# Performance work log

Measured on AMD Instinct MI355X. Metric: run time of the kernel, lower is better.

Reference implementation:

```python
import jax, jax.numpy as jnp
import numpy as np

H, R, B = 8192, 4, 64


def glorot(key, shape):
    return jax.random.uniform(key, shape, minval=-1.0, maxval=1.0) * jnp.sqrt(2.0 / sum(shape))


def setup_inputs() -> dict:
    key = jax.random.key(0)
    k1, k2, k3, k4, kh, kx = jax.random.split(key, 6)
    return {
        "h": jax.random.normal(kh, (B, H), dtype=jnp.float32),
        "x": jax.random.normal(kx, (B, H), dtype=jnp.float32),
        "a_diag": glorot(k1, (H,)).astype(jnp.float32),
        "p_vec": glorot(k2, (H, R)).astype(jnp.float32),
        "q_vec": glorot(k3, (H, R)).astype(jnp.float32),
        "b_mat": glorot(k4, (H, H)).astype(jnp.float32),
    }


def reference(h, x, a_diag, p_vec, q_vec, b_mat):
    # Faithful to the source: explicitly materialize the dense DPLR matrix
    # a_dplr = diag(a_diag) + p q^T  (H x H), then a_dplr @ h + b_mat.T @ x.
    a_dplr = jnp.diag(a_diag) + p_vec @ q_vec.T  # (H, H)
    # Batched over leading dim: (a_dplr @ h_i) == h @ a_dplr.T ; (b_mat.T @ x_i) == x @ b_mat
    return h @ a_dplr.T + x @ b_mat  # (B, H)
```

## Files before the change

kernel.cpp:

```cpp
#include <hip/hip_runtime.h>
#include <hip/hip_bf16.h>


#define HDIM 8192
#define BDIM 64
#define RDIM 4
#define KSPLIT 16
#define KSLAB 512
#define NKTILE (KSLAB / 32)

typedef short short8 __attribute__((ext_vector_type(8)));
typedef float f32x2 __attribute__((ext_vector_type(2)));
typedef float f32x4 __attribute__((ext_vector_type(4)));
typedef float f32x16 __attribute__((ext_vector_type(16)));

__device__ __forceinline__ unsigned f2bf(float f) {
  unsigned u = __float_as_uint(f);
  unsigned r = u + 0x7fffu + ((u >> 16) & 1u);
  return r >> 16;
}

__device__ __forceinline__ float bf2f(unsigned short u) {
  return __uint_as_float(((unsigned)u) << 16);
}

__global__ __launch_bounds__(256)
void prep_hq_kernel(const float* __restrict__ x,
                    const float* __restrict__ h,
                    const float* __restrict__ q,
                    unsigned short* __restrict__ xb,
                    float* __restrict__ hq) {
  const int b = blockIdx.x, t = threadIdx.x;
  {
    const float* xrow = x + (size_t)b * HDIM;
    unsigned short* xo = xb + (size_t)b * HDIM;
#pragma unroll
    for (int i = 0; i < 4; ++i) {
      const int base = (t * 4 + i) * 8;
      f32x4 v0 = *(const f32x4*)(xrow + base);
      f32x4 v1 = *(const f32x4*)(xrow + base + 4);
      union { unsigned short u[8]; short8 s; } o;
#pragma unroll
      for (int e = 0; e < 4; ++e) {
        o.u[e] = (unsigned short)f2bf(v0[e]);
        o.u[4 + e] = (unsigned short)f2bf(v1[e]);
      }
      *(short8*)(xo + base) = o.s;
    }
  }
  const float* hrow = h + (size_t)b * HDIM;
  f32x4 s = {0.f, 0.f, 0.f, 0.f};
  for (int k = t; k < HDIM; k += 256) {
    float hv = hrow[k];
    f32x4 qv = *(const f32x4*)(q + (size_t)k * RDIM);
    s += hv * qv;
  }
  __shared__ f32x4 red[256];
  red[t] = s;
  __syncthreads();
  for (int off = 128; off > 0; off >>= 1) {
    if (t < off) red[t] += red[t + off];
    __syncthreads();
  }
  if (t == 0) *(f32x4*)(hq + (size_t)b * RDIM) = red[0];
}

__global__ __launch_bounds__(512, 2)
void dplr_main(const float* __restrict__ bmat,
               const unsigned short* __restrict__ xb,
               unsigned short* __restrict__ part) {
  __shared__ __align__(16) unsigned short xs[BDIM * KSLAB];

  const int t    = threadIdx.x;
  const int lane = t & 63;
  const int w    = t >> 6;
  const int c32  = lane & 31;
  const int kh   = lane >> 5;

  const int jg = blockIdx.x & 15;
  const int ks = blockIdx.x >> 4;
  const int k0 = ks * KSLAB;

  {
    const int row = t >> 3;
    const int g0  = (t & 7) * 8;
    const unsigned short* src = xb + (size_t)row * HDIM + k0 + g0 * 8;
#pragma unroll
    for (int i = 0; i < 8; ++i) {
      const int g  = row * (KSLAB / 8) + g0 + i;
      const int gs = g ^ (row & 7);
      *(short8*)&xs[gs * 8] = *(const short8*)(src + i * 8);
    }
  }
  __syncthreads();

  const int j0 = jg * 512 + w * 64;
  const float* b0 = bmat + (size_t)(k0 + kh * 8) * HDIM + j0 + 2 * c32;

  f32x16 acc[2][2];
#pragma unroll
  for (int mt = 0; mt < 2; ++mt)
#pragma unroll
    for (int n = 0; n < 2; ++n)
#pragma unroll
      for (int r = 0; r < 16; ++r) acc[mt][n][r] = 0.f;

  f32x2 LA[16], LB[16], LC[16], LD[16];

  auto issue = [&](int kt, f32x2* L) {
#pragma unroll
    for (int s = 0; s < 2; ++s)
#pragma unroll
      for (int i = 0; i < 8; ++i)
        L[s * 8 + i] = *(const f32x2*)(b0 + (size_t)(kt * 32 + s * 16 + i) * HDIM);
  };

  auto conv_mfma = [&](int kt, const f32x2* L) {
#pragma unroll
    for (int s = 0; s < 2; ++s) {
      union { unsigned u[4]; short8 v; } bf0, bf1;
#pragma unroll
      for (int j = 0; j < 4; ++j) {
        const f32x2 a = L[s * 8 + 2 * j];
        const f32x2 b = L[s * 8 + 2 * j + 1];
        bf0.u[j] = f2bf(a.x) | (f2bf(b.x) << 16);
        bf1.u[j] = f2bf(a.y) | (f2bf(b.y) << 16);
      }
#pragma unroll
      for (int mt = 0; mt < 2; ++mt) {
        const int row = mt * 32 + c32;
        const int g   = row * (KSLAB / 8) + kt * 4 + s * 2 + kh;
        const int gs  = g ^ (row & 7);
        short8 af = *(const short8*)&xs[gs * 8];
        acc[mt][0] = __builtin_amdgcn_mfma_f32_32x32x16_bf16(af, bf0.v, acc[mt][0], 0, 0, 0);
        acc[mt][1] = __builtin_amdgcn_mfma_f32_32x32x16_bf16(af, bf1.v, acc[mt][1], 0, 0, 0);
      }
    }
  };

  issue(0, LA);
  issue(1, LB);
  issue(2, LC);
  issue(3, LD);
  for (int kt = 0; kt < NKTILE; kt += 4) {
    conv_mfma(kt, LA);
    if (kt + 4 < NKTILE) issue(kt + 4, LA);
    conv_mfma(kt + 1, LB);
    if (kt + 5 < NKTILE) issue(kt + 5, LB);
    conv_mfma(kt + 2, LC);
    if (kt + 6 < NKTILE) issue(kt + 6, LC);
    conv_mfma(kt + 3, LD);
    if (kt + 7 < NKTILE) issue(kt + 7, LD);
  }

  unsigned short* pb = part + (size_t)ks * BDIM * HDIM;
#pragma unroll
  for (int mt = 0; mt < 2; ++mt)
#pragma unroll
    for (int n = 0; n < 2; ++n)
#pragma unroll
      for (int reg = 0; reg < 16; ++reg) {
        const int row = mt * 32 + (reg & 3) + 8 * (reg >> 2) + 4 * kh;
        const int col = j0 + 2 * c32 + n;
        pb[(size_t)row * HDIM + col] = (unsigned short)f2bf(acc[mt][n][reg]);
      }
}

__global__ __launch_bounds__(256)
void combine_kernel(const unsigned short* __restrict__ part,
                    const float* __restrict__ h,
                    const float* __restrict__ adiag,
                    const float* __restrict__ pvec,
                    const float* __restrict__ hq,
                    float* __restrict__ out) {
  const int tid  = blockIdx.x * 256 + threadIdx.x;
  const int base = tid * 8;
  const int row  = base >> 13;
  const int j    = base & 8191;

  float s[8];
#pragma unroll
  for (int e = 0; e < 8; ++e) s[e] = 0.f;
  const unsigned short* pp = part + (size_t)row * HDIM + j;
#pragma unroll
  for (int ks = 0; ks < KSPLIT; ++ks) {
    union { unsigned short u[8]; short8 v; } pv;
    pv.v = *(const short8*)(pp + (size_t)ks * BDIM * HDIM);
#pragma unroll
    for (int e = 0; e < 8; ++e) s[e] += bf2f(pv.u[e]);
  }
  const f32x4 hv0 = *(const f32x4*)(h + (size_t)row * HDIM + j);
  const f32x4 hv1 = *(const f32x4*)(h + (size_t)row * HDIM + j + 4);
  const f32x4 a0  = *(const f32x4*)(adiag + j);
  const f32x4 a1  = *(const f32x4*)(adiag + j + 4);
  const f32x4 hqv = *(const f32x4*)(hq + (size_t)row * RDIM);

  float res[8];
#pragma unroll
  for (int e = 0; e < 4; ++e) {
    const f32x4 pv = *(const f32x4*)(pvec + (size_t)(j + e) * RDIM);
    res[e] = s[e] + hv0[e] * a0[e] +
             hqv[0] * pv[0] + hqv[1] * pv[1] + hqv[2] * pv[2] + hqv[3] * pv[3];
  }
#pragma unroll
  for (int e = 0; e < 4; ++e) {
    const f32x4 pv = *(const f32x4*)(pvec + (size_t)(j + 4 + e) * RDIM);
    res[4 + e] = s[4 + e] + hv1[e] * a1[e] +
                 hqv[0] * pv[0] + hqv[1] * pv[1] + hqv[2] * pv[2] + hqv[3] * pv[3];
  }
  f32x4 o0 = {res[0], res[1], res[2], res[3]};
  f32x4 o1 = {res[4], res[5], res[6], res[7]};
  *(f32x4*)(out + (size_t)row * HDIM + j) = o0;
  *(f32x4*)(out + (size_t)row * HDIM + j + 4) = o1;
}

extern "C" void kernel_launch(void* const* d_in, const int* in_sizes, int n_in,
                              void* d_out, int out_size, void* d_ws, size_t ws_size,
                              hipStream_t stream) {
  const float* h     = (const float*)d_in[0];
  const float* x     = (const float*)d_in[1];
  const float* adiag = (const float*)d_in[2];
  const float* pvec  = (const float*)d_in[3];
  const float* qvec  = (const float*)d_in[4];
  const float* bmat  = (const float*)d_in[5];
  float* out = (float*)d_out;

  unsigned short* xb = (unsigned short*)d_ws;
  float* hqbuf = (float*)((char*)d_ws + ((size_t)1 << 20));
  unsigned short* part = (unsigned short*)((char*)d_ws + ((size_t)2 << 20));

  prep_hq_kernel<<<BDIM, 256, 0, stream>>>(x, h, qvec, xb, hqbuf);
  dplr_main<<<KSPLIT * 16, 512, 0, stream>>>(bmat, xb, part);
  combine_kernel<<<(BDIM * HDIM / 8) / 256, 256, 0, stream>>>(part, h, adiag, pvec, hqbuf, out);
}
```

Before: 73.53 us.

## Widen B-tile per wave, convert x inside main kernel, double K-split

The main GEMM kernel now converts fp32 x to bf16 directly into shared memory, so the separate x-conversion pass and its workspace buffer go away. Each wave loads full 128-byte-per-lane-pair rows of b_mat and uses v_permlane32_swap to rearrange them into MFMA operands, covering 128 output columns with 4 accumulators instead of 64 with 2. K is split 32 ways with 256-deep slabs, keeping the grid at 256 blocks. The cost is twice as many partial-sum slabs for the combine kernel to read and more accumulator registers per wave.

```diff
diff --git a/kernel.cpp b/kernel.cpp
--- a/kernel.cpp
+++ b/kernel.cpp
@@ -5,9 +5,9 @@
 #define HDIM 8192
 #define BDIM 64
 #define RDIM 4
-#define KSPLIT 16
-#define KSLAB 512
-#define NKTILE (KSLAB / 32)
+#define KSPLIT 32
+#define KSLAB 256
+#define NSTEP (KSLAB / 16)
 
 typedef short short8 __attribute__((ext_vector_type(8)));
 typedef float f32x2 __attribute__((ext_vector_type(2)));
@@ -25,29 +25,10 @@
 }
 
 __global__ __launch_bounds__(256)
-void prep_hq_kernel(const float* __restrict__ x,
-                    const float* __restrict__ h,
-                    const float* __restrict__ q,
-                    unsigned short* __restrict__ xb,
-                    float* __restrict__ hq) {
+void hq_kernel(const float* __restrict__ h,
+               const float* __restrict__ q,
+               float* __restrict__ hq) {
   const int b = blockIdx.x, t = threadIdx.x;
-  {
-    const float* xrow = x + (size_t)b * HDIM;
-    unsigned short* xo = xb + (size_t)b * HDIM;
-#pragma unroll
-    for (int i = 0; i < 4; ++i) {
-      const int base = (t * 4 + i) * 8;
-      f32x4 v0 = *(const f32x4*)(xrow + base);
-      f32x4 v1 = *(const f32x4*)(xrow + base + 4);
-      union { unsigned short u[8]; short8 s; } o;
-#pragma unroll
-      for (int e = 0; e < 4; ++e) {
-        o.u[e] = (unsigned short)f2bf(v0[e]);
-        o.u[4 + e] = (unsigned short)f2bf(v1[e]);
-      }
-      *(short8*)(xo + base) = o.s;
-    }
-  }
   const float* hrow = h + (size_t)b * HDIM;
   f32x4 s = {0.f, 0.f, 0.f, 0.f};
   for (int k = t; k < HDIM; k += 256) {
@@ -67,7 +48,7 @@
 
 __global__ __launch_bounds__(512, 2)
 void dplr_main(const float* __restrict__ bmat,
-               const unsigned short* __restrict__ xb,
+               const float* __restrict__ x,
                unsigned short* __restrict__ part) {
   __shared__ __align__(16) unsigned short xs[BDIM * KSLAB];
 
@@ -77,93 +58,100 @@
   const int c32  = lane & 31;
   const int kh   = lane >> 5;
 
-  const int jg = blockIdx.x & 15;
-  const int ks = blockIdx.x >> 4;
+  const int jg = blockIdx.x & 7;
+  const int ks = blockIdx.x >> 3;
   const int k0 = ks * KSLAB;
 
   {
-    const int row = t >> 3;
-    const int g0  = (t & 7) * 8;
-    const unsigned short* src = xb + (size_t)row * HDIM + k0 + g0 * 8;
+    const int row  = t >> 3;
+    const int koff = (t & 7) * 32;
+    const float* src = x + (size_t)row * HDIM + k0 + koff;
+#pragma unroll
+    for (int i = 0; i < 4; ++i) {
+      f32x4 va = *(const f32x4*)(src + i * 8);
+      f32x4 vb = *(const f32x4*)(src + i * 8 + 4);
+      union { unsigned short u[8]; short8 s; } o;
+#pragma unroll
+      for (int e = 0; e < 4; ++e) {
+        o.u[e]     = (unsigned short)f2bf(va[e]);
+        o.u[4 + e] = (unsigned short)f2bf(vb[e]);
+      }
+      const int g  = row * (KSLAB / 8) + (t & 7) * 4 + i;
+      const int gs = g ^ (row & 7);
+      *(short8*)&xs[gs * 8] = o.s;
+    }
+  }
+  __syncthreads();
+
+  const int j0 = jg * 1024 + w * 128;
+  const float* b0 = bmat + (size_t)k0 * HDIM + j0 + 2 * lane;
+
+  f32x16 acc[2][4];
+#pragma unroll
+  for (int mt = 0; mt < 2; ++mt)
+#pragma unroll
+    for (int n = 0; n < 4; ++n)
+#pragma unroll
+      for (int r = 0; r < 16; ++r) acc[mt][n][r] = 0.f;
+
+  f32x2 LA[16], LB[16];
+
+  auto issue = [&](int kt, f32x2* L) {
+#pragma unroll
+    for (int i = 0; i < 16; ++i)
+      L[i] = *(const f32x2*)(b0 + (size_t)(kt * 16 + i) * HDIM);
+  };
+
+  auto consume = [&](int kt, f32x2* L) {
 #pragma unroll
     for (int i = 0; i < 8; ++i) {
-      const int g  = row * (KSLAB / 8) + g0 + i;
-      const int gs = g ^ (row & 7);
-      *(short8*)&xs[gs * 8] = *(const short8*)(src + i * 8);
-    }
-  }
-  __syncthreads();
-
-  const int j0 = jg * 512 + w * 64;
-  const float* b0 = bmat + (size_t)(k0 + kh * 8) * HDIM + j0 + 2 * c32;
-
-  f32x16 acc[2][2];
-#pragma unroll
-  for (int mt = 0; mt < 2; ++mt)
-#pragma unroll
-    for (int n = 0; n < 2; ++n)
-#pragma unroll
-      for (int r = 0; r < 16; ++r) acc[mt][n][r] = 0.f;
-
-  f32x2 LA[16], LB[16], LC[16], LD[16];
-
-  auto issue = [&](int kt, f32x2* L) {
-#pragma unroll
-    for (int s = 0; s < 2; ++s)
-#pragma unroll
-      for (int i = 0; i < 8; ++i)
-        L[s * 8 + i] = *(const f32x2*)(b0 + (size_t)(kt * 32 + s * 16 + i) * HDIM);
-  };
-
-  auto conv_mfma = [&](int kt, const f32x2* L) {
-#pragma unroll
-    for (int s = 0; s < 2; ++s) {
-      union { unsigned u[4]; short8 v; } bf0, bf1;
-#pragma unroll
-      for (int j = 0; j < 4; ++j) {
-        const f32x2 a = L[s * 8 + 2 * j];
-        const f32x2 b = L[s * 8 + 2 * j + 1];
-        bf0.u[j] = f2bf(a.x) | (f2bf(b.x) << 16);
-        bf1.u[j] = f2bf(a.y) | (f2bf(b.y) << 16);
-      }
-#pragma unroll
-      for (int mt = 0; mt < 2; ++mt) {
-        const int row = mt * 32 + c32;
-        const int g   = row * (KSLAB / 8) + kt * 4 + s * 2 + kh;
-        const int gs  = g ^ (row & 7);
-        short8 af = *(const short8*)&xs[gs * 8];
-        acc[mt][0] = __builtin_amdgcn_mfma_f32_32x32x16_bf16(af, bf0.v, acc[mt][0], 0, 0, 0);
-        acc[mt][1] = __builtin_amdgcn_mfma_f32_32x32x16_bf16(af, bf1.v, acc[mt][1], 0, 0, 0);
-      }
+      asm volatile("v_permlane32_swap_b32 %0, %1"
+                   : "+v"(L[i].x), "+v"(L[i + 8].x));
+      asm volatile("v_permlane32_swap_b32 %0, %1"
+                   : "+v"(L[i].y), "+v"(L[i + 8].y));
+    }
+    union { unsigned u[4]; short8 v; } bf[4];
+#pragma unroll
+    for (int j = 0; j < 4; ++j) {
+      bf[0].u[j] = f2bf(L[2 * j].x)     | (f2bf(L[2 * j + 1].x) << 16);
+      bf[1].u[j] = f2bf(L[2 * j].y)     | (f2bf(L[2 * j + 1].y) << 16);
+      bf[2].u[j] = f2bf(L[8 + 2 * j].x) | (f2bf(L[8 + 2 * j + 1].x) << 16);
+      bf[3].u[j] = f2bf(L[8 + 2 * j].y) | (f2bf(L[8 + 2 * j + 1].y) << 16);
+    }
+#pragma unroll
+    for (int mt = 0; mt < 2; ++mt) {
+      const int row = mt * 32 + c32;
+      const int g   = row * (KSLAB / 8) + kt * 2 + kh;
+      const int gs  = g ^ (row & 7);
+      short8 af = *(const short8*)&xs[gs * 8];
+#pragma unroll
+      for (int n = 0; n < 4; ++n)
+        acc[mt][n] =
+            __builtin_amdgcn_mfma_f32_32x32x16_bf16(af, bf[n].v, acc[mt][n], 0, 0, 0);
     }
   };
 
   issue(0, LA);
   issue(1, LB);
-  issue(2, LC);
-  issue(3, LD);
-  for (int kt = 0; kt < NKTILE; kt += 4) {
-    conv_mfma(kt, LA);
-    if (kt + 4 < NKTILE) issue(kt + 4, LA);
-    conv_mfma(kt + 1, LB);
-    if (kt + 5 < NKTILE) issue(kt + 5, LB);
-    conv_mfma(kt + 2, LC);
-    if (kt + 6 < NKTILE) issue(kt + 6, LC);
-    conv_mfma(kt + 3, LD);
-    if (kt + 7 < NKTILE) issue(kt + 7, LD);
+  for (int kt = 0; kt < NSTEP; kt += 2) {
+    consume(kt, LA);
+    if (kt + 2 < NSTEP) issue(kt + 2, LA);
+    consume(kt + 1, LB);
+    if (kt + 3 < NSTEP) issue(kt + 3, LB);
   }
 
   unsigned short* pb = part + (size_t)ks * BDIM * HDIM;
 #pragma unroll
   for (int mt = 0; mt < 2; ++mt)
 #pragma unroll
-    for (int n = 0; n < 2; ++n)
+    for (int n = 0; n < 4; ++n) {
+      const int col = j0 + ((n >> 1) * 64) + 2 * c32 + (n & 1);
 #pragma unroll
       for (int reg = 0; reg < 16; ++reg) {
         const int row = mt * 32 + (reg & 3) + 8 * (reg >> 2) + 4 * kh;
-        const int col = j0 + 2 * c32 + n;
         pb[(size_t)row * HDIM + col] = (unsigned short)f2bf(acc[mt][n][reg]);
       }
+    }
 }
 
 __global__ __launch_bounds__(256)
@@ -225,11 +213,10 @@
   const float* bmat  = (const float*)d_in[5];
   float* out = (float*)d_out;
 
-  unsigned short* xb = (unsigned short*)d_ws;
-  float* hqbuf = (float*)((char*)d_ws + ((size_t)1 << 20));
-  unsigned short* part = (unsigned short*)((char*)d_ws + ((size_t)2 << 20));
-
-  prep_hq_kernel<<<BDIM, 256, 0, stream>>>(x, h, qvec, xb, hqbuf);
-  dplr_main<<<KSPLIT * 16, 512, 0, stream>>>(bmat, xb, part);
+  float* hqbuf = (float*)d_ws;
+  unsigned short* part = (unsigned short*)((char*)d_ws + ((size_t)1 << 20));
+
+  hq_kernel<<<BDIM, 256, 0, stream>>>(h, qvec, hqbuf);
+  dplr_main<<<KSPLIT * 8, 512, 0, stream>>>(bmat, x, part);
   combine_kernel<<<(BDIM * HDIM / 8) / 256, 256, 0, stream>>>(part, h, adiag, pvec, hqbuf, out);
 }
```

After: 77.75 us. +5.7%, slower.
